# Kernel tuning notes

Hardware: AMD Instinct MI355X
Metric: run time of the kernel (lower is better)

## Reference

```python
import jax, jax.numpy as jnp
import numpy as np

N, F_IN, UNITS, HEADS = 4096, 128, 64, 4
EDGE_P = 0.01  # adjacency density


def setup_inputs() -> dict:
    key = jax.random.key(0)
    k1, k2, k3, k4, k5 = jax.random.split(key, 5)
    inputs = jax.random.normal(k1, (N, F_IN), dtype=jnp.float32)
    adj = jax.random.bernoulli(k2, EDGE_P, (N, N)).astype(jnp.float32)
    # glorot-normal-ish parameter scales
    w = jax.random.normal(k3, (F_IN, UNITS), dtype=jnp.float32) * np.float32(np.sqrt(2.0 / (F_IN + UNITS)))
    attn_w1 = jax.random.normal(k4, (UNITS, HEADS), dtype=jnp.float32) * np.float32(np.sqrt(2.0 / (UNITS + HEADS)))
    attn_w2 = jax.random.normal(k5, (UNITS, HEADS), dtype=jnp.float32) * np.float32(np.sqrt(2.0 / (UNITS + HEADS)))
    return {"inputs": inputs, "adj": adj, "w": w, "attn_w1": attn_w1, "attn_w2": attn_w2}


def reference(inputs, adj, w, attn_w1, attn_w2):
    # dropout=0, bias=0, final_layer=False, activation=relu
    x = inputs @ w                                  # [N, U]
    e1 = x @ attn_w1                                # [N, H]
    e2 = x @ attn_w2                                # [N, H]
    # coeffs[i, j, h] = relu(e1[i, h] + e2[j, h])
    coeffs = jax.nn.relu(e1[:, None, :] + e2[None, :, :])   # [N, N, H]
    # NOTE: original multiplies by adj (zeros -> logit 0, not -inf) then softmax over j
    scores = adj[:, :, None] * coeffs               # [N, N, H]
    attn = jax.nn.softmax(scores, axis=1)           # normalize over neighbors j
    # per-head aggregation, concat heads -> [N, H*U] (head-major blocks)
    out = jnp.einsum("ijh,ju->ihu", attn, x).reshape(N, HEADS * UNITS)
    return jax.nn.relu(out)
```

## Files before the change

### kernel.cpp

```cpp
#include <hip/hip_runtime.h>
#include <hip/hip_bf16.h>

#define N_NODES 4096
#define F_IN    128
#define UNITS   64
#define HEADS   4
#define WT_PITCH 132
#define CHUNK   64
#define CAP     160

__global__ __launch_bounds__(256) void kA(const float* __restrict__ inputs,
                                          const float* __restrict__ adj,
                                          const float* __restrict__ w,
                                          const float* __restrict__ aw1,
                                          const float* __restrict__ aw2,
                                          float* __restrict__ x,
                                          float* __restrict__ e1,
                                          float* __restrict__ e2,
                                          float* __restrict__ partial,
                                          int* __restrict__ cnt_ws,
                                          unsigned short* __restrict__ nbr_ws) {
    __shared__ union {
        struct {
            float w_t[UNITS * WT_PITCH];
            float in_lds[16 * F_IN];
            float x_lds[16 * 65];
            float aw_lds[2 * UNITS * HEADS];
        } g;
        struct {
            unsigned short nbr_l[CAP];
            int cnt;
        } s;
    } sm;

    const int t = threadIdx.x;

    if (blockIdx.x < 256) {
        const int b = blockIdx.x;
        const int row0 = b * 16;

        for (int idx = t; idx < F_IN * UNITS; idx += 256) {
            const int u = idx & 63;
            const int k = idx >> 6;
            sm.g.w_t[u * WT_PITCH + k] = w[idx];
        }
        {
            const float4* src = (const float4*)(inputs + (size_t)row0 * F_IN);
            float4* dst = (float4*)sm.g.in_lds;
            for (int idx = t; idx < 16 * F_IN / 4; idx += 256) dst[idx] = src[idx];
        }
        if (t < UNITS * HEADS) {
            sm.g.aw_lds[t] = aw1[t];
            sm.g.aw_lds[UNITS * HEADS + t] = aw2[t];
        }
        __syncthreads();

        const int u = t & 63;
        const int rg = t >> 6;
        float acc0 = 0.f, acc1 = 0.f, acc2 = 0.f, acc3 = 0.f;
        const float4* wrow = (const float4*)(sm.g.w_t + u * WT_PITCH);
        const float4* i0 = (const float4*)(sm.g.in_lds + (rg * 4 + 0) * F_IN);
        const float4* i1 = (const float4*)(sm.g.in_lds + (rg * 4 + 1) * F_IN);
        const float4* i2 = (const float4*)(sm.g.in_lds + (rg * 4 + 2) * F_IN);
        const float4* i3 = (const float4*)(sm.g.in_lds + (rg * 4 + 3) * F_IN);
#pragma unroll 8
        for (int c = 0; c < F_IN / 4; c++) {
            const float4 wv = wrow[c];
            float4 v;
            v = i0[c]; acc0 = fmaf(wv.x, v.x, fmaf(wv.y, v.y, fmaf(wv.z, v.z, fmaf(wv.w, v.w, acc0))));
            v = i1[c]; acc1 = fmaf(wv.x, v.x, fmaf(wv.y, v.y, fmaf(wv.z, v.z, fmaf(wv.w, v.w, acc1))));
            v = i2[c]; acc2 = fmaf(wv.x, v.x, fmaf(wv.y, v.y, fmaf(wv.z, v.z, fmaf(wv.w, v.w, acc2))));
            v = i3[c]; acc3 = fmaf(wv.x, v.x, fmaf(wv.y, v.y, fmaf(wv.z, v.z, fmaf(wv.w, v.w, acc3))));
        }
        sm.g.x_lds[(rg * 4 + 0) * 65 + u] = acc0;
        sm.g.x_lds[(rg * 4 + 1) * 65 + u] = acc1;
        sm.g.x_lds[(rg * 4 + 2) * 65 + u] = acc2;
        sm.g.x_lds[(rg * 4 + 3) * 65 + u] = acc3;
        x[(size_t)(row0 + rg * 4 + 0) * UNITS + u] = acc0;
        x[(size_t)(row0 + rg * 4 + 1) * UNITS + u] = acc1;
        x[(size_t)(row0 + rg * 4 + 2) * UNITS + u] = acc2;
        x[(size_t)(row0 + rg * 4 + 3) * UNITS + u] = acc3;
        __syncthreads();

        if (t < 128) {
            const int r = t >> 3;
            const int rem = t & 7;
            const int h = rem & 3;
            const bool first = rem < 4;
            const float* aw = sm.g.aw_lds + (first ? 0 : UNITS * HEADS);
            float s = 0.f;
#pragma unroll 8
            for (int uu = 0; uu < UNITS; uu++)
                s += sm.g.x_lds[r * 65 + uu] * aw[uu * HEADS + h];
            (first ? e1 : e2)[(size_t)(row0 + r) * HEADS + h] = s;
        }

        if (t < 64) {
            float s = 0.f;
#pragma unroll
            for (int r = 0; r < 16; r++) s += sm.g.x_lds[r * 65 + t];
            partial[b * 64 + t] = s;
        }
    } else {
        const int i = blockIdx.x - 256;
        if (t == 0) sm.s.cnt = 0;
        __syncthreads();

        const float4* arow = (const float4*)(adj + (size_t)i * N_NODES);
        const float4 v0 = arow[t];
        const float4 v1 = arow[t + 256];
        const float4 v2 = arow[t + 512];
        const float4 v3 = arow[t + 768];

#define EMIT(val, col) if ((val) != 0.f) { int _i = atomicAdd(&sm.s.cnt, 1); if (_i < CAP) sm.s.nbr_l[_i] = (unsigned short)(col); }
        {
            const int b0 = t * 4;
            EMIT(v0.x, b0 + 0) EMIT(v0.y, b0 + 1) EMIT(v0.z, b0 + 2) EMIT(v0.w, b0 + 3)
            const int b1 = (t + 256) * 4;
            EMIT(v1.x, b1 + 0) EMIT(v1.y, b1 + 1) EMIT(v1.z, b1 + 2) EMIT(v1.w, b1 + 3)
            const int b2 = (t + 512) * 4;
            EMIT(v2.x, b2 + 0) EMIT(v2.y, b2 + 1) EMIT(v2.z, b2 + 2) EMIT(v2.w, b2 + 3)
            const int b3 = (t + 768) * 4;
            EMIT(v3.x, b3 + 0) EMIT(v3.y, b3 + 1) EMIT(v3.z, b3 + 2) EMIT(v3.w, b3 + 3)
        }
#undef EMIT
        __syncthreads();

        const int m = min(sm.s.cnt, CAP);
        if (t == 0) cnt_ws[i] = m;
        if (t < m) nbr_ws[(size_t)i * CAP + t] = sm.s.nbr_l[t];
    }
}

__global__ __launch_bounds__(256) void kB(const float* __restrict__ partial,
                                          float* __restrict__ S) {
    __shared__ float red[4][64];
    const int u = threadIdx.x & 63;
    const int q = threadIdx.x >> 6;
    float s = 0.f;
#pragma unroll 8
    for (int b = q; b < 256; b += 4) s += partial[b * 64 + u];
    red[q][u] = s;
    __syncthreads();
    if (threadIdx.x < 64) S[u] = red[0][u] + red[1][u] + red[2][u] + red[3][u];
}

__global__ __launch_bounds__(256) void kC(const float* __restrict__ x,
                                          const float* __restrict__ e1,
                                          const float* __restrict__ e2,
                                          const float* __restrict__ S,
                                          const int* __restrict__ cnt_ws,
                                          const unsigned short* __restrict__ nbr_ws,
                                          float* __restrict__ out) {
    __shared__ unsigned short nbr[CAP];
    __shared__ float xs[CHUNK * UNITS];
    __shared__ float wgt[CHUNK * 4];

    const int i = blockIdx.x;
    const int t = threadIdx.x;

    const int n = cnt_ws[i];
    if (t < n) nbr[t] = nbr_ws[(size_t)i * CAP + t];
    __syncthreads();

    const int h = t >> 6;
    const int u = t & 63;

    const float4 e1v = *(const float4*)(e1 + (size_t)i * HEADS);

    float acc = 0.f;
    float den = 0.f;

    for (int base = 0; base < n; base += CHUNK) {
        const int m = min(n - base, CHUNK);

        if (t < m) {
            const int j = nbr[base + t];
            const float4 e2v = *(const float4*)(e2 + (size_t)j * HEADS);
            float4 wv;
            wv.x = __expf(fmaxf(e1v.x + e2v.x, 0.f)) - 1.f;
            wv.y = __expf(fmaxf(e1v.y + e2v.y, 0.f)) - 1.f;
            wv.z = __expf(fmaxf(e1v.z + e2v.z, 0.f)) - 1.f;
            wv.w = __expf(fmaxf(e1v.w + e2v.w, 0.f)) - 1.f;
            *(float4*)(wgt + t * 4) = wv;
        }
        for (int idx = t; idx < m * UNITS; idx += 256) {
            const int k = idx >> 6;
            const int uu = idx & 63;
            xs[idx] = x[(size_t)nbr[base + k] * UNITS + uu];
        }
        __syncthreads();

#pragma unroll 8
        for (int k = 0; k < m; k++) {
            const float wv = wgt[k * 4 + h];
            den += wv;
            acc = fmaf(wv, xs[k * UNITS + u], acc);
        }
        __syncthreads();
    }

    const float numer = S[u] + acc;
    const float denom = (float)N_NODES + den;
    out[(size_t)i * (HEADS * UNITS) + t] = fmaxf(numer / denom, 0.f);
}

extern "C" void kernel_launch(void* const* d_in, const int* in_sizes, int n_in,
                              void* d_out, int out_size, void* d_ws, size_t ws_size,
                              hipStream_t stream) {
    const float* inputs = (const float*)d_in[0];
    const float* adj    = (const float*)d_in[1];
    const float* w      = (const float*)d_in[2];
    const float* aw1    = (const float*)d_in[3];
    const float* aw2    = (const float*)d_in[4];
    float* out = (float*)d_out;

    float* ws = (float*)d_ws;
    float* x       = ws;
    float* e1      = ws + 262144;
    float* e2      = ws + 262144 + 16384;
    float* partial = ws + 262144 + 2 * 16384;
    float* S       = ws + 262144 + 3 * 16384;
    int* cnt_ws    = (int*)(S + 64);
    unsigned short* nbr_ws = (unsigned short*)(cnt_ws + N_NODES);

    kA<<<256 + N_NODES, 256, 0, stream>>>(inputs, adj, w, aw1, aw2,
                                          x, e1, e2, partial, cnt_ws, nbr_ws);
    kB<<<1, 256, 0, stream>>>(partial, S);
    kC<<<N_NODES, 256, 0, stream>>>(x, e1, e2, S, cnt_ws, nbr_ws, out);
}
```

Before: 120.6 us.

## Fuse three kernels into one cooperative kernel with grid sync

Merges the projection/neighbor-extraction kernel, the partial-sum reduction kernel and the aggregation kernel into a single cooperative launch of 512 blocks, separated by a grid-wide barrier. The column sum S is now accumulated with global atomics after a memset instead of a separate reduction kernel. Each block handles 16 adjacency rows in phase one and 8 output rows in phase two, which removes two launch gaps but cuts parallelism from 4096 blocks to 512 and serializes row processing inside blocks. It also adds the grid.sync cost.

After: 230.6 us. +91.3%, slower.

```diff
diff --git a/kernel.cpp b/kernel.cpp
--- a/kernel.cpp
+++ b/kernel.cpp
@@ -1,5 +1,8 @@
 #include <hip/hip_runtime.h>
 #include <hip/hip_bf16.h>
+#include <hip/hip_cooperative_groups.h>
+
+namespace cg = cooperative_groups;
 
 #define N_NODES 4096
 #define F_IN    128
@@ -8,18 +11,22 @@
 #define WT_PITCH 132
 #define CHUNK   64
 #define CAP     160
-
-__global__ __launch_bounds__(256) void kA(const float* __restrict__ inputs,
-                                          const float* __restrict__ adj,
-                                          const float* __restrict__ w,
-                                          const float* __restrict__ aw1,
-                                          const float* __restrict__ aw2,
-                                          float* __restrict__ x,
-                                          float* __restrict__ e1,
-                                          float* __restrict__ e2,
-                                          float* __restrict__ partial,
-                                          int* __restrict__ cnt_ws,
-                                          unsigned short* __restrict__ nbr_ws) {
+#define GRID    512
+
+__global__ __launch_bounds__(256) void mega(const float* __restrict__ inputs,
+                                            const float* __restrict__ adj,
+                                            const float* __restrict__ w,
+                                            const float* __restrict__ aw1,
+                                            const float* __restrict__ aw2,
+                                            float* __restrict__ x,
+                                            float* __restrict__ e1,
+                                            float* __restrict__ e2,
+                                            float* __restrict__ S,
+                                            int* __restrict__ cnt_ws,
+                                            unsigned short* __restrict__ nbr_ws,
+                                            float* __restrict__ out) {
+    cg::grid_group grid = cg::this_grid();
+
     __shared__ union {
         struct {
             float w_t[UNITS * WT_PITCH];
@@ -31,13 +38,18 @@
             unsigned short nbr_l[CAP];
             int cnt;
         } s;
+        struct {
+            unsigned short nbr[CAP];
+            float xs[CHUNK * UNITS];
+            float wgt[CHUNK * 4];
+        } c;
     } sm;
 
     const int t = threadIdx.x;
-
-    if (blockIdx.x < 256) {
-        const int b = blockIdx.x;
-        const int row0 = b * 16;
+    const int bid = blockIdx.x;
+
+    if (bid < 256) {
+        const int row0 = bid * 16;
 
         for (int idx = t; idx < F_IN * UNITS; idx += 256) {
             const int u = idx & 63;
@@ -99,110 +111,89 @@
             float s = 0.f;
 #pragma unroll
             for (int r = 0; r < 16; r++) s += sm.g.x_lds[r * 65 + t];
-            partial[b * 64 + t] = s;
+            atomicAdd(&S[t], s);
         }
     } else {
-        const int i = blockIdx.x - 256;
-        if (t == 0) sm.s.cnt = 0;
-        __syncthreads();
-
-        const float4* arow = (const float4*)(adj + (size_t)i * N_NODES);
-        const float4 v0 = arow[t];
-        const float4 v1 = arow[t + 256];
-        const float4 v2 = arow[t + 512];
-        const float4 v3 = arow[t + 768];
-
+        for (int rr = 0; rr < 16; rr++) {
+            const int r = (bid - 256) * 16 + rr;
+            if (t == 0) sm.s.cnt = 0;
+            __syncthreads();
+
+            const float4* arow = (const float4*)(adj + (size_t)r * N_NODES);
+            const float4 v0 = arow[t];
+            const float4 v1 = arow[t + 256];
+            const float4 v2 = arow[t + 512];
+            const float4 v3 = arow[t + 768];
 #define EMIT(val, col) if ((val) != 0.f) { int _i = atomicAdd(&sm.s.cnt, 1); if (_i < CAP) sm.s.nbr_l[_i] = (unsigned short)(col); }
-        {
-            const int b0 = t * 4;
-            EMIT(v0.x, b0 + 0) EMIT(v0.y, b0 + 1) EMIT(v0.z, b0 + 2) EMIT(v0.w, b0 + 3)
-            const int b1 = (t + 256) * 4;
-            EMIT(v1.x, b1 + 0) EMIT(v1.y, b1 + 1) EMIT(v1.z, b1 + 2) EMIT(v1.w, b1 + 3)
-            const int b2 = (t + 512) * 4;
-            EMIT(v2.x, b2 + 0) EMIT(v2.y, b2 + 1) EMIT(v2.z, b2 + 2) EMIT(v2.w, b2 + 3)
-            const int b3 = (t + 768) * 4;
-            EMIT(v3.x, b3 + 0) EMIT(v3.y, b3 + 1) EMIT(v3.z, b3 + 2) EMIT(v3.w, b3 + 3)
-        }
+            {
+                const int b0 = t * 4;
+                EMIT(v0.x, b0 + 0) EMIT(v0.y, b0 + 1) EMIT(v0.z, b0 + 2) EMIT(v0.w, b0 + 3)
+                const int b1 = (t + 256) * 4;
+                EMIT(v1.x, b1 + 0) EMIT(v1.y, b1 + 1) EMIT(v1.z, b1 + 2) EMIT(v1.w, b1 + 3)
+                const int b2 = (t + 512) * 4;
+                EMIT(v2.x, b2 + 0) EMIT(v2.y, b2 + 1) EMIT(v2.z, b2 + 2) EMIT(v2.w, b2 + 3)
+                const int b3 = (t + 768) * 4;
+                EMIT(v3.x, b3 + 0) EMIT(v3.y, b3 + 1) EMIT(v3.z, b3 + 2) EMIT(v3.w, b3 + 3)
+            }
 #undef EMIT
-        __syncthreads();
-
-        const int m = min(sm.s.cnt, CAP);
-        if (t == 0) cnt_ws[i] = m;
-        if (t < m) nbr_ws[(size_t)i * CAP + t] = sm.s.nbr_l[t];
+            __syncthreads();
+            const int m = min(sm.s.cnt, CAP);
+            __syncthreads();
+            if (t == 0) cnt_ws[r] = m;
+            if (t < m) nbr_ws[(size_t)r * CAP + t] = sm.s.nbr_l[t];
+        }
     }
-}
-
-__global__ __launch_bounds__(256) void kB(const float* __restrict__ partial,
-                                          float* __restrict__ S) {
-    __shared__ float red[4][64];
-    const int u = threadIdx.x & 63;
-    const int q = threadIdx.x >> 6;
-    float s = 0.f;
-#pragma unroll 8
-    for (int b = q; b < 256; b += 4) s += partial[b * 64 + u];
-    red[q][u] = s;
-    __syncthreads();
-    if (threadIdx.x < 64) S[u] = red[0][u] + red[1][u] + red[2][u] + red[3][u];
-}
-
-__global__ __launch_bounds__(256) void kC(const float* __restrict__ x,
-                                          const float* __restrict__ e1,
-                                          const float* __restrict__ e2,
-                                          const float* __restrict__ S,
-                                          const int* __restrict__ cnt_ws,
-                                          const unsigned short* __restrict__ nbr_ws,
-                                          float* __restrict__ out) {
-    __shared__ unsigned short nbr[CAP];
-    __shared__ float xs[CHUNK * UNITS];
-    __shared__ float wgt[CHUNK * 4];
-
-    const int i = blockIdx.x;
-    const int t = threadIdx.x;
-
-    const int n = cnt_ws[i];
-    if (t < n) nbr[t] = nbr_ws[(size_t)i * CAP + t];
-    __syncthreads();
+
+    grid.sync();
 
     const int h = t >> 6;
     const int u = t & 63;
-
-    const float4 e1v = *(const float4*)(e1 + (size_t)i * HEADS);
-
-    float acc = 0.f;
-    float den = 0.f;
-
-    for (int base = 0; base < n; base += CHUNK) {
-        const int m = min(n - base, CHUNK);
-
-        if (t < m) {
-            const int j = nbr[base + t];
-            const float4 e2v = *(const float4*)(e2 + (size_t)j * HEADS);
-            float4 wv;
-            wv.x = __expf(fmaxf(e1v.x + e2v.x, 0.f)) - 1.f;
-            wv.y = __expf(fmaxf(e1v.y + e2v.y, 0.f)) - 1.f;
-            wv.z = __expf(fmaxf(e1v.z + e2v.z, 0.f)) - 1.f;
-            wv.w = __expf(fmaxf(e1v.w + e2v.w, 0.f)) - 1.f;
-            *(float4*)(wgt + t * 4) = wv;
-        }
-        for (int idx = t; idx < m * UNITS; idx += 256) {
-            const int k = idx >> 6;
-            const int uu = idx & 63;
-            xs[idx] = x[(size_t)nbr[base + k] * UNITS + uu];
-        }
-        __syncthreads();
+    const float Sv = S[u];
+
+    for (int rr = 0; rr < 8; rr++) {
+        const int i = bid * 8 + rr;
+        const int n = cnt_ws[i];
+        if (t < n) sm.c.nbr[t] = nbr_ws[(size_t)i * CAP + t];
+        __syncthreads();
+
+        const float4 e1v = *(const float4*)(e1 + (size_t)i * HEADS);
+
+        float acc = 0.f;
+        float den = 0.f;
+
+        for (int base = 0; base < n; base += CHUNK) {
+            const int m = min(n - base, CHUNK);
+
+            if (t < m) {
+                const int j = sm.c.nbr[base + t];
+                const float4 e2v = *(const float4*)(e2 + (size_t)j * HEADS);
+                float4 wv;
+                wv.x = __expf(fmaxf(e1v.x + e2v.x, 0.f)) - 1.f;
+                wv.y = __expf(fmaxf(e1v.y + e2v.y, 0.f)) - 1.f;
+                wv.z = __expf(fmaxf(e1v.z + e2v.z, 0.f)) - 1.f;
+                wv.w = __expf(fmaxf(e1v.w + e2v.w, 0.f)) - 1.f;
+                *(float4*)(sm.c.wgt + t * 4) = wv;
+            }
+            for (int idx = t; idx < m * UNITS; idx += 256) {
+                const int k = idx >> 6;
+                const int uu = idx & 63;
+                sm.c.xs[idx] = x[(size_t)sm.c.nbr[base + k] * UNITS + uu];
+            }
+            __syncthreads();
 
 #pragma unroll 8
-        for (int k = 0; k < m; k++) {
-            const float wv = wgt[k * 4 + h];
-            den += wv;
-            acc = fmaf(wv, xs[k * UNITS + u], acc);
-        }
+            for (int k = 0; k < m; k++) {
+                const float wv = sm.c.wgt[k * 4 + h];
+                den += wv;
+                acc = fmaf(wv, sm.c.xs[k * UNITS + u], acc);
+            }
+            __syncthreads();
+        }
+
+        out[(size_t)i * (HEADS * UNITS) + t] =
+            fmaxf((Sv + acc) / ((float)N_NODES + den), 0.f);
         __syncthreads();
     }
-
-    const float numer = S[u] + acc;
-    const float denom = (float)N_NODES + den;
-    out[(size_t)i * (HEADS * UNITS) + t] = fmaxf(numer / denom, 0.f);
 }
 
 extern "C" void kernel_launch(void* const* d_in, const int* in_sizes, int n_in,
@@ -216,16 +207,18 @@
     float* out = (float*)d_out;
 
     float* ws = (float*)d_ws;
-    float* x       = ws;
-    float* e1      = ws + 262144;
-    float* e2      = ws + 262144 + 16384;
-    float* partial = ws + 262144 + 2 * 16384;
-    float* S       = ws + 262144 + 3 * 16384;
-    int* cnt_ws    = (int*)(S + 64);
+    float* x  = ws;
+    float* e1 = ws + 262144;
+    float* e2 = ws + 262144 + 16384;
+    float* S  = ws + 262144 + 2 * 16384;
+    int* cnt_ws = (int*)(S + 64);
     unsigned short* nbr_ws = (unsigned short*)(cnt_ws + N_NODES);
 
-    kA<<<256 + N_NODES, 256, 0, stream>>>(inputs, adj, w, aw1, aw2,
-                                          x, e1, e2, partial, cnt_ws, nbr_ws);
-    kB<<<1, 256, 0, stream>>>(partial, S);
-    kC<<<N_NODES, 256, 0, stream>>>(x, e1, e2, S, cnt_ws, nbr_ws, out);
+    hipMemsetAsync(S, 0, 64 * sizeof(float), stream);
+
+    void* args[] = {(void*)&inputs, (void*)&adj, (void*)&w, (void*)&aw1, (void*)&aw2,
+                    (void*)&x, (void*)&e1, (void*)&e2, (void*)&S,
+                    (void*)&cnt_ws, (void*)&nbr_ws, (void*)&out};
+    hipLaunchCooperativeKernel((const void*)mega, dim3(GRID), dim3(256),
+                               args, 0, stream);
 }
```
